# Performance work log

Hardware: AMD Instinct MI355X
Metric: run time of the kernel (lower is better)

Reference implementation:

```python
import jax, jax.numpy as jnp
import numpy as np

BETA = 0.9
TH = 1.0
SLOPE = 25.0  # fast-sigmoid surrogate slope (spike_grad_slope)

@jax.custom_vjp
def spike_fn(m):
    # Heaviside on (mem - threshold)
    return (m > 0).astype(m.dtype)

def _spike_fwd(m):
    return spike_fn(m), m

def _spike_bwd(m, g):
    # fast-sigmoid surrogate gradient: 1 / (slope*|m| + 1)^2
    return (g / (SLOPE * jnp.abs(m) + 1.0) ** 2,)

spike_fn.defvjp(_spike_fwd, _spike_bwd)


def setup_inputs() -> dict:
    key = jax.random.key(0)
    k1, k2, k3 = jax.random.split(key, 3)
    T, B, I, H, O = 128, 8192, 2, 256, 2
    x = jax.random.normal(k1, (T, B, I), dtype=jnp.float32)
    # xavier_uniform with gain=1: limit = sqrt(6/(fan_in+fan_out))
    lim1 = float(np.sqrt(6.0 / (I + H)))
    lim2 = float(np.sqrt(6.0 / (H + O)))
    W1 = jax.random.uniform(k2, (H, I), jnp.float32, -lim1, lim1)
    W2 = jax.random.uniform(k3, (O, H), jnp.float32, -lim2, lim2)
    return {"x": x, "W1": W1, "W2": W2}


def reference(x, W1, W2):
    # Precompute all per-step input currents in one GEMM: [T,B,H]
    cur = jnp.einsum('tbi,hi->tbh', x, W1)
    B, H = cur.shape[1], cur.shape[2]
    mem0 = jnp.zeros((B, H), cur.dtype)

    def step(mem, c):
        # snntorch Leaky (reset_mechanism='subtract'):
        # reset based on PREVIOUS mem's spike, then leaky integrate, then fire
        reset = spike_fn(mem - TH)
        mem_new = BETA * mem + c - reset * TH
        spk = spike_fn(mem_new - TH)
        # original code detaches mem between steps (1-step truncated BPTT)
        return jax.lax.stop_gradient(mem_new), spk

    _, spk_rec = jax.lax.scan(step, mem0, cur)  # spk_rec: [T,B,H]
    spk_avg = spk_rec[-10:].mean(0)             # [B,H]
    out = jnp.einsum('bh,oh->bo', spk_avg, W2)  # [B,O]
    return out
```

## Files before the change

kernel.cpp:

```cpp
#include <hip/hip_runtime.h>


#define T_STEPS 128
#define BATCH   8192
#define IN_N    2
#define HID     256
#define OUT_N   2
#define TAIL    10
#define R       8

__global__ __launch_bounds__(256) void snn_fwd(const float* __restrict__ x,
                                               const float* __restrict__ W1,
                                               const float* __restrict__ W2,
                                               float* __restrict__ out) {
    const int h  = threadIdx.x;
    const int b0 = blockIdx.x * R;

    const float w0 = W1[2 * h];
    const float w1 = W1[2 * h + 1];

    const float* xb = x + (size_t)blockIdx.x * (R * IN_N);

    float mem[R], spk[R], cnt[R];
#pragma unroll
    for (int r = 0; r < R; ++r) { mem[r] = 0.0f; spk[r] = 0.0f; cnt[r] = 0.0f; }

#define STEP(r, xa, xb_)                                                         \
    {                                                                            \
        const float c = __fadd_rn(__fmul_rn((xa), w0), __fmul_rn((xb_), w1));    \
        mem[r] = __fsub_rn(__fadd_rn(__fmul_rn(0.9f, mem[r]), c), spk[r]);       \
        spk[r] = (mem[r] > 1.0f) ? 1.0f : 0.0f;                                  \
    }

#pragma unroll 4
    for (int t = 0; t < T_STEPS - TAIL; ++t) {
        const float* xt = xb + (size_t)t * (BATCH * IN_N);
        float xv[R * IN_N];
#pragma unroll
        for (int k = 0; k < R * IN_N; ++k) xv[k] = xt[k];
#pragma unroll
        for (int r = 0; r < R; ++r) STEP(r, xv[2 * r], xv[2 * r + 1])
    }
#pragma unroll 2
    for (int t = T_STEPS - TAIL; t < T_STEPS; ++t) {
        const float* xt = xb + (size_t)t * (BATCH * IN_N);
        float xv[R * IN_N];
#pragma unroll
        for (int k = 0; k < R * IN_N; ++k) xv[k] = xt[k];
#pragma unroll
        for (int r = 0; r < R; ++r) {
            STEP(r, xv[2 * r], xv[2 * r + 1])
            cnt[r] += spk[r];
        }
    }
#undef STEP

    const float w2a = W2[h];
    const float w2b = W2[HID + h];
    float p0[R], p1[R];
#pragma unroll
    for (int r = 0; r < R; ++r) {
        const float avg = cnt[r] / 10.0f;
        p0[r] = avg * w2a;
        p1[r] = avg * w2b;
    }

#pragma unroll
    for (int off = 32; off > 0; off >>= 1) {
#pragma unroll
        for (int r = 0; r < R; ++r) {
            p0[r] += __shfl_down(p0[r], off, 64);
            p1[r] += __shfl_down(p1[r], off, 64);
        }
    }

    __shared__ float red[4][R][OUT_N];
    const int wave = h >> 6;
    const int lane = h & 63;
    if (lane == 0) {
#pragma unroll
        for (int r = 0; r < R; ++r) { red[wave][r][0] = p0[r]; red[wave][r][1] = p1[r]; }
    }
    __syncthreads();
    if (h < R * OUT_N) {
        const int r = h >> 1, o = h & 1;
        out[(size_t)(b0 + r) * OUT_N + o] =
            (red[0][r][o] + red[1][r][o]) + (red[2][r][o] + red[3][r][o]);
    }
}

extern "C" void kernel_launch(void* const* d_in, const int* in_sizes, int n_in,
                              void* d_out, int out_size, void* d_ws, size_t ws_size,
                              hipStream_t stream) {
    const float* x  = (const float*)d_in[0];
    const float* W1 = (const float*)d_in[1];
    const float* W2 = (const float*)d_in[2];
    float* out = (float*)d_out;

    snn_fwd<<<BATCH / R, HID, 0, stream>>>(x, W1, W2, out);
}
```

Baseline: 113.8 us.

## Remap threads to batch lanes with hidden units per thread and split reduction

Each lane now owns one batch element and a wave handles 8 hidden units, so every thread reads a single coalesced float2 per timestep instead of 16 broadcast scalar loads. Hidden units are split across 8 block groups, each writing per-batch partial sums to workspace, and a second kernel sums those partials. This is meant to remove the redundant, uncoalesced x loads and the shuffle-heavy reduction. The cost is an extra kernel launch and a workspace round trip.

```diff
diff --git a/kernel.cpp b/kernel.cpp
--- a/kernel.cpp
+++ b/kernel.cpp
@@ -3,90 +3,94 @@
 
 #define T_STEPS 128
 #define BATCH   8192
-#define IN_N    2
 #define HID     256
-#define OUT_N   2
 #define TAIL    10
-#define R       8
+#define RH      8
+#define LB      64
+#define NWAVE   4
+#define HG      8
 
-__global__ __launch_bounds__(256) void snn_fwd(const float* __restrict__ x,
-                                               const float* __restrict__ W1,
-                                               const float* __restrict__ W2,
-                                               float* __restrict__ out) {
-    const int h  = threadIdx.x;
-    const int b0 = blockIdx.x * R;
+__global__ __launch_bounds__(256) void snn_scan(const float* __restrict__ x,
+                                                const float* __restrict__ W1,
+                                                const float* __restrict__ W2,
+                                                float2* __restrict__ partial) {
+    const int tid   = threadIdx.x;
+    const int lane  = tid & 63;
+    const int wave  = tid >> 6;
+    const int hg    = blockIdx.x & (HG - 1);
+    const int bg    = blockIdx.x >> 3;
+    const int b     = bg * LB + lane;
+    const int hbase = hg * (NWAVE * RH) + wave * RH;
 
-    const float w0 = W1[2 * h];
-    const float w1 = W1[2 * h + 1];
+    float w0[RH], w1[RH];
+#pragma unroll
+    for (int r = 0; r < RH; ++r) {
+        w0[r] = W1[2 * (hbase + r)];
+        w1[r] = W1[2 * (hbase + r) + 1];
+    }
 
-    const float* xb = x + (size_t)blockIdx.x * (R * IN_N);
+    const float2* xb = (const float2*)x + b;
 
-    float mem[R], spk[R], cnt[R];
+    float mem[RH], spk[RH], cnt[RH];
 #pragma unroll
-    for (int r = 0; r < R; ++r) { mem[r] = 0.0f; spk[r] = 0.0f; cnt[r] = 0.0f; }
+    for (int r = 0; r < RH; ++r) { mem[r] = 0.0f; spk[r] = 0.0f; cnt[r] = 0.0f; }
 
-#define STEP(r, xa, xb_)                                                         \
+#define STEP(r, xa, xc)                                                          \
     {                                                                            \
-        const float c = __fadd_rn(__fmul_rn((xa), w0), __fmul_rn((xb_), w1));    \
+        const float c = __fadd_rn(__fmul_rn((xa), w0[r]), __fmul_rn((xc), w1[r]));\
         mem[r] = __fsub_rn(__fadd_rn(__fmul_rn(0.9f, mem[r]), c), spk[r]);       \
         spk[r] = (mem[r] > 1.0f) ? 1.0f : 0.0f;                                  \
     }
 
 #pragma unroll 4
     for (int t = 0; t < T_STEPS - TAIL; ++t) {
-        const float* xt = xb + (size_t)t * (BATCH * IN_N);
-        float xv[R * IN_N];
+        const float2 xv = xb[(size_t)t * BATCH];
 #pragma unroll
-        for (int k = 0; k < R * IN_N; ++k) xv[k] = xt[k];
+        for (int r = 0; r < RH; ++r) STEP(r, xv.x, xv.y)
+    }
 #pragma unroll
-        for (int r = 0; r < R; ++r) STEP(r, xv[2 * r], xv[2 * r + 1])
-    }
-#pragma unroll 2
     for (int t = T_STEPS - TAIL; t < T_STEPS; ++t) {
-        const float* xt = xb + (size_t)t * (BATCH * IN_N);
-        float xv[R * IN_N];
+        const float2 xv = xb[(size_t)t * BATCH];
 #pragma unroll
-        for (int k = 0; k < R * IN_N; ++k) xv[k] = xt[k];
-#pragma unroll
-        for (int r = 0; r < R; ++r) {
-            STEP(r, xv[2 * r], xv[2 * r + 1])
+        for (int r = 0; r < RH; ++r) {
+            STEP(r, xv.x, xv.y)
             cnt[r] += spk[r];
         }
     }
 #undef STEP
 
-    const float w2a = W2[h];
-    const float w2b = W2[HID + h];
-    float p0[R], p1[R];
+    float p0 = 0.0f, p1 = 0.0f;
 #pragma unroll
-    for (int r = 0; r < R; ++r) {
+    for (int r = 0; r < RH; ++r) {
         const float avg = cnt[r] / 10.0f;
-        p0[r] = avg * w2a;
-        p1[r] = avg * w2b;
+        p0 = __fadd_rn(p0, __fmul_rn(avg, W2[hbase + r]));
+        p1 = __fadd_rn(p1, __fmul_rn(avg, W2[HID + hbase + r]));
     }
 
+    __shared__ float2 red[NWAVE][LB];
+    red[wave][lane] = make_float2(p0, p1);
+    __syncthreads();
+    if (wave == 0) {
+        const float2 a0 = red[0][lane], a1 = red[1][lane];
+        const float2 a2 = red[2][lane], a3 = red[3][lane];
+        float2 s;
+        s.x = __fadd_rn(__fadd_rn(a0.x, a1.x), __fadd_rn(a2.x, a3.x));
+        s.y = __fadd_rn(__fadd_rn(a0.y, a1.y), __fadd_rn(a2.y, a3.y));
+        partial[(size_t)hg * BATCH + b] = s;
+    }
+}
+
+__global__ __launch_bounds__(256) void snn_reduce(const float2* __restrict__ partial,
+                                                  float2* __restrict__ out) {
+    const int b = blockIdx.x * 256 + threadIdx.x;
+    float sx = 0.0f, sy = 0.0f;
 #pragma unroll
-    for (int off = 32; off > 0; off >>= 1) {
-#pragma unroll
-        for (int r = 0; r < R; ++r) {
-            p0[r] += __shfl_down(p0[r], off, 64);
-            p1[r] += __shfl_down(p1[r], off, 64);
-        }
+    for (int hg = 0; hg < HG; ++hg) {
+        const float2 p = partial[(size_t)hg * BATCH + b];
+        sx = __fadd_rn(sx, p.x);
+        sy = __fadd_rn(sy, p.y);
     }
-
-    __shared__ float red[4][R][OUT_N];
-    const int wave = h >> 6;
-    const int lane = h & 63;
-    if (lane == 0) {
-#pragma unroll
-        for (int r = 0; r < R; ++r) { red[wave][r][0] = p0[r]; red[wave][r][1] = p1[r]; }
-    }
-    __syncthreads();
-    if (h < R * OUT_N) {
-        const int r = h >> 1, o = h & 1;
-        out[(size_t)(b0 + r) * OUT_N + o] =
-            (red[0][r][o] + red[1][r][o]) + (red[2][r][o] + red[3][r][o]);
-    }
+    out[b] = make_float2(sx, sy);
 }
 
 extern "C" void kernel_launch(void* const* d_in, const int* in_sizes, int n_in,
@@ -95,7 +99,9 @@
     const float* x  = (const float*)d_in[0];
     const float* W1 = (const float*)d_in[1];
     const float* W2 = (const float*)d_in[2];
-    float* out = (float*)d_out;
+    float2* out     = (float2*)d_out;
+    float2* partial = (float2*)d_ws;
 
-    snn_fwd<<<BATCH / R, HID, 0, stream>>>(x, W1, W2, out);
+    snn_scan<<<(BATCH / LB) * HG, 256, 0, stream>>>(x, W1, W2, partial);
+    snn_reduce<<<BATCH / 256, 256, 0, stream>>>(partial, out);
 }
```

Result: faster. 105.1 us (-7.7%).
